# Performance work log

Measured on AMD Instinct MI355X. Metric: run time of the kernel, lower is better.

Reference implementation:

```python
import jax, jax.numpy as jnp
import numpy as np

EPS = 1e-08

def rotate_half(x):
    # split last dim into 2 halves: '... (j d) -> ... j d', j=2
    x1, x2 = jnp.split(x, 2, axis=-1)
    return jnp.concatenate((-x2, x1), axis=-1)

def apply_rotary_pos_emb(t, freqs):
    seq_len = t.shape[-2]
    freqs = freqs[:, :, -seq_len:]
    return t * jnp.cos(freqs) + rotate_half(t) * jnp.sin(freqs)

def setup_inputs() -> dict:
    key = jax.random.key(0)
    ks = jax.random.split(key, 6)
    B, N, D, H, DH = 2, 2048, 1024, 16, 64
    inner = H * DH
    x = jax.random.normal(ks[0], (B, N, D), dtype=jnp.float32)
    # realistic rotary frequencies over dim_head
    inv_freq = 1.0 / (10000.0 ** (np.arange(0, DH, 2, dtype=np.float32) / DH))
    t = np.arange(N, dtype=np.float32)
    freqs = np.einsum('n,f->nf', t, inv_freq)            # [N, DH/2]
    pos_emb = jnp.asarray(np.concatenate([freqs, freqs], axis=-1)[None, None])  # [1,1,N,DH]
    gamma = jnp.ones((D,), dtype=jnp.float32)
    Wq = jax.random.normal(ks[1], (D, inner), dtype=jnp.float32) * (D ** -0.5)
    Wkv = jax.random.normal(ks[2], (D, 2 * inner), dtype=jnp.float32) * (D ** -0.5)
    Wo = jax.random.normal(ks[3], (inner, D), dtype=jnp.float32) * (inner ** -0.5)
    bo = jnp.zeros((D,), dtype=jnp.float32)
    return {"x": x, "pos_emb": pos_emb, "gamma": gamma, "Wq": Wq, "Wkv": Wkv, "Wo": Wo, "bo": bo}

def reference(x, pos_emb, gamma, Wq, Wkv, Wo, bo):
    B, N, D = x.shape
    H = 16
    DH = Wq.shape[1] // H
    scale = DH ** -0.5
    # NOTE: kv_input is the UN-normalized x (captured before RMSNorm in the original)
    kv_input = x
    # RMSNorm: x / clamp(||x|| * dim^-0.5, eps) * gamma
    norm = jnp.linalg.norm(x, axis=-1, keepdims=True) * (D ** -0.5)
    xn = x / jnp.maximum(norm, EPS) * gamma
    q = xn @ Wq                                   # [B,N,H*DH]
    kv = kv_input @ Wkv
    k, v = jnp.split(kv, 2, axis=-1)
    def to_heads(t):
        return t.reshape(B, N, H, DH).transpose(0, 2, 1, 3)  # b h n d
    q, k, v = to_heads(q), to_heads(k), to_heads(v)
    q = q * scale
    q = apply_rotary_pos_emb(q, pos_emb)
    k = apply_rotary_pos_emb(k, pos_emb)
    sim = jnp.einsum('bhid,bhjd->bhij', q, k)
    i, j = sim.shape[-2:]
    causal_mask = jnp.triu(jnp.ones((i, j), dtype=bool), k=j - i + 1)
    mask_value = -jnp.finfo(sim.dtype).max
    sim = jnp.where(causal_mask, mask_value, sim)
    attn = jax.nn.softmax(sim, axis=-1)
    out = jnp.einsum('bhij,bhjd->bhid', attn, v)
    out = out.transpose(0, 2, 1, 3).reshape(B, N, H * DH)
    return out @ Wo + bo
```

## Files before the change

### kernel.cpp

```cpp
#include <hip/hip_runtime.h>
#include <cmath>

#define B_ 2
#define N_ 2048
#define D_ 1024
#define H_ 16

typedef __attribute__((ext_vector_type(8))) short short8;
typedef __attribute__((ext_vector_type(4))) float f32x4;
typedef __attribute__((ext_vector_type(4))) unsigned short u16x4;
typedef __attribute__((ext_vector_type(4))) unsigned int uint4v;

__device__ __forceinline__ unsigned short f2bf(float f) {
    union { float f; unsigned u; } x;
    x.f = f;
    unsigned r = x.u + 0x7FFFu + ((x.u >> 16) & 1u);
    return (unsigned short)(r >> 16);
}
__device__ __forceinline__ float bf2f(unsigned short u) {
    union { unsigned u; float f; } x;
    x.u = ((unsigned)u) << 16;
    return x.f;
}
__device__ __forceinline__ unsigned cvt_pk_bf16(float lo, float hi) {
    unsigned r;
    asm("v_cvt_pk_bf16_f32 %0, %1, %2" : "=v"(r) : "v"(lo), "v"(hi));
    return r;
}
__device__ __forceinline__ float exp2_fast(float x) {
    float r;
    asm("v_exp_f32 %0, %1" : "=v"(r) : "v"(x));
    return r;
}
__device__ __forceinline__ void gload_lds16(const void* g, void* l) {
    __builtin_amdgcn_global_load_lds((const __attribute__((address_space(1))) unsigned*)g,
                                     (__attribute__((address_space(3))) unsigned*)l,
                                     16, 0, 0);
}

__global__ __launch_bounds__(256) void freqtab_kernel(const float* __restrict__ pos,
                                                      float2* __restrict__ tabq,
                                                      float2* __restrict__ tabk) {
    const int idx = blockIdx.x * 256 + threadIdx.x;
    const float f = pos[idx];
    const float cc = cosf(f), ss = sinf(f);
    const float sq = 0.125f * 1.4426950408889634f;
    tabq[idx] = make_float2(sq * cc, sq * ss);
    tabk[idx] = make_float2(cc, ss);
}

__global__ __launch_bounds__(256) void rmsnorm_kernel(const float* __restrict__ x,
                                                      unsigned short* __restrict__ xb,
                                                      float* __restrict__ s) {
    const int row = blockIdx.x;
    const float4 v = reinterpret_cast<const float4*>(x + (size_t)row * D_)[threadIdx.x];
    float ss = v.x * v.x + v.y * v.y + v.z * v.z + v.w * v.w;
    #pragma unroll
    for (int off = 32; off; off >>= 1) ss += __shfl_xor(ss, off, 64);
    __shared__ float wss[4];
    if ((threadIdx.x & 63) == 0) wss[threadIdx.x >> 6] = ss;
    __syncthreads();
    const float tot = wss[0] + wss[1] + wss[2] + wss[3];
    const float inv = 1.0f / fmaxf(sqrtf(tot * (1.0f / D_)), 1e-8f);
    if (threadIdx.x == 0) s[row] = inv;
    u16x4 ox;
    ox[0] = f2bf(v.x); ox[1] = f2bf(v.y); ox[2] = f2bf(v.z); ox[3] = f2bf(v.w);
    *reinterpret_cast<u16x4*>(xb + (size_t)row * D_ + threadIdx.x * 4) = ox;
}

__global__ __launch_bounds__(256) void convT_all_kernel(const float* __restrict__ Wq,
                                                        const float* __restrict__ Wkv,
                                                        const float* __restrict__ Wo,
                                                        const float* __restrict__ gamma,
                                                        unsigned short* __restrict__ Wqt,
                                                        unsigned short* __restrict__ Wkvt,
                                                        unsigned short* __restrict__ Wot) {
    __shared__ float tile[32][33];
    const int bx = blockIdx.x;
    const float* W;
    unsigned short* Wt;
    int Nm, n0;
    bool gmul = false;
    if (bx < 32)       { W = Wq;  Wt = Wqt;  Nm = 1024; n0 = bx * 32; gmul = true; }
    else if (bx < 96)  { W = Wkv; Wt = Wkvt; Nm = 2048; n0 = (bx - 32) * 32; }
    else               { W = Wo;  Wt = Wot;  Nm = 1024; n0 = (bx - 96) * 32; }
    const int k0 = blockIdx.y * 32;
    const int r = threadIdx.x >> 3, c4 = (threadIdx.x & 7) * 4;
    const float4 ld = *reinterpret_cast<const float4*>(W + (size_t)(k0 + r) * Nm + n0 + c4);
    tile[r][c4 + 0] = ld.x; tile[r][c4 + 1] = ld.y;
    tile[r][c4 + 2] = ld.z; tile[r][c4 + 3] = ld.w;
    __syncthreads();
    u16x4 o;
    #pragma unroll
    for (int j = 0; j < 4; ++j) {
        float v = tile[c4 + j][r];
        if (gmul) v *= gamma[k0 + c4 + j];
        o[j] = f2bf(v);
    }
    *reinterpret_cast<u16x4*>(Wt + (size_t)(n0 + r) * 1024 + k0 + c4) = o;
}

__global__ __launch_bounds__(256) void gemm_qkv_kernel(const unsigned short* __restrict__ xb,
                                                       const unsigned short* __restrict__ Wqt,
                                                       const unsigned short* __restrict__ Wkvt,
                                                       const float* __restrict__ s,
                                                       unsigned short* __restrict__ qb,
                                                       unsigned short* __restrict__ kb,
                                                       unsigned short* __restrict__ vt,
                                                       const float2* __restrict__ tabq,
                                                       const float2* __restrict__ tabk) {
    __shared__ unsigned short As[2][64 * 64];
    __shared__ unsigned short Bs[2][128 * 64];
    __shared__ float sld[64];
    const int bid = blockIdx.x;
    const int xcd = bid & 7;
    const int ii = bid >> 3;
    const int bx = xcd * 3 + (ii % 3);
    const int m0 = (ii / 3) * 64;

    const unsigned short* Bt;
    int n0;
    if (bx < 8)       { Bt = Wqt;  n0 = bx * 128; }
    else if (bx < 16) { Bt = Wkvt; n0 = (bx - 8) * 128; }
    else              { Bt = Wkvt; n0 = (bx - 16) * 128 + 1024; }

    const int tid = threadIdx.x, lane = tid & 63, w = tid >> 6;
    const int wm = w >> 1, wn = w & 1;
    const int cc = lane & 15;
    const int sr = tid >> 3;
    const int sc = (tid & 7) * 8;

    if (tid < 64) sld[tid] = s[m0 + tid];

    f32x4 acc[2][4] = {};

    #pragma unroll
    for (int i = 0; i < 4; ++i) {
        const int r = i * 32 + sr;
        const int cs = sc ^ ((r & 7) << 3);
        if (i < 2)
            gload_lds16(xb + (size_t)(m0 + r) * 1024 + cs, (char*)As[0] + i * 4096 + w * 1024);
        gload_lds16(Bt + (size_t)(n0 + r) * 1024 + cs, (char*)Bs[0] + i * 4096 + w * 1024);
    }

    for (int t = 0; t < 16; ++t) {
        if (t + 1 < 16) {
            const int k0 = (t + 1) * 64;
            char* ad = (char*)As[(t + 1) & 1];
            char* bd = (char*)Bs[(t + 1) & 1];
            #pragma unroll
            for (int i = 0; i < 4; ++i) {
                const int r = i * 32 + sr;
                const int cs = sc ^ ((r & 7) << 3);
                if (i < 2)
                    gload_lds16(xb + (size_t)(m0 + r) * 1024 + k0 + cs, ad + i * 4096 + w * 1024);
                gload_lds16(Bt + (size_t)(n0 + r) * 1024 + k0 + cs, bd + i * 4096 + w * 1024);
            }
            asm volatile("s_waitcnt vmcnt(6)" ::: "memory");
        } else {
            asm volatile("s_waitcnt vmcnt(0)" ::: "memory");
        }
        __builtin_amdgcn_s_barrier();

        const char* Ac = (const char*)As[t & 1];
        const char* Bc = (const char*)Bs[t & 1];

        short8 af[2][2], bf[4][2];
        #pragma unroll
        for (int mf = 0; mf < 2; ++mf)
            #pragma unroll
            for (int ks = 0; ks < 2; ++ks) {
                const int r = wm * 32 + mf * 16 + cc;
                const int cb = (ks * 64 + ((lane >> 4) * 16)) ^ ((r & 7) << 4);
                af[mf][ks] = *reinterpret_cast<const short8*>(Ac + r * 128 + cb);
            }
        #pragma unroll
        for (int nf = 0; nf < 4; ++nf)
            #pragma unroll
            for (int ks = 0; ks < 2; ++ks) {
                const int r = wn * 64 + nf * 16 + cc;
                const int cb = (ks * 64 + ((lane >> 4) * 16)) ^ ((r & 7) << 4);
                bf[nf][ks] = *reinterpret_cast<const short8*>(Bc + r * 128 + cb);
            }
        #pragma unroll
        for (int ks = 0; ks < 2; ++ks)
            #pragma unroll
            for (int mf = 0; mf < 2; ++mf)
                #pragma unroll
                for (int nf = 0; nf < 4; ++nf)
                    acc[mf][nf] = __builtin_amdgcn_mfma_f32_16x16x32_bf16(af[mf][ks], bf[nf][ks], acc[mf][nf], 0, 0, 0);

        __builtin_amdgcn_s_barrier();
    }

    if (bx < 16) {
        const float2* tab = (bx < 8) ? tabq : tabk;
        unsigned short* dst = (bx < 8) ? qb : kb;
        const bool doscale = (bx < 8);
        #pragma unroll
        for (int mf = 0; mf < 2; ++mf)
            #pragma unroll
            for (int reg = 0; reg < 4; ++reg) {
                const int rloc = wm * 32 + mf * 16 + (lane >> 4) * 4 + reg;
                const int row = m0 + rloc;
                const int n = row & (N_ - 1);
                const float srow = doscale ? sld[rloc] : 1.0f;
                #pragma unroll
                for (int nf = 0; nf < 2; ++nf) {
                    const int d = nf * 16 + cc;
                    const float2 t1 = tab[n * 64 + d];
                    const float2 t2 = tab[n * 64 + 32 + d];
                    const float x1 = acc[mf][nf][reg] * srow;
                    const float x2 = acc[mf][nf + 2][reg] * srow;
                    const float o1 = x1 * t1.x - x2 * t1.y;
                    const float o2 = x2 * t2.x + x1 * t2.y;
                    const int col = n0 + wn * 64 + nf * 16 + cc;
                    dst[(size_t)row * 1024 + col] = f2bf(o1);
                    dst[(size_t)row * 1024 + col + 32] = f2bf(o2);
                }
            }
    } else {
        const int bb = m0 >> 11;
        const int gg = lane >> 4;
        const int tb = m0 & (N_ - 1);
        #pragma unroll
        for (int mf = 0; mf < 2; ++mf) {
            const int npos = tb + wm * 32 + (gg >> 1) * 16 + (gg & 1) * 8 + mf * 4;
            #pragma unroll
            for (int nf = 0; nf < 4; ++nf) {
                const int cv = n0 - 1024 + wn * 64 + nf * 16 + cc;
                const int h = cv >> 6, d = cv & 63;
                uint2 u;
                u.x = cvt_pk_bf16(acc[mf][nf][0], acc[mf][nf][1]);
                u.y = cvt_pk_bf16(acc[mf][nf][2], acc[mf][nf][3]);
                *reinterpret_cast<uint2*>(vt + ((size_t)(bb * 16 + h) * 64 + d) * 2048 + npos) = u;
            }
        }
    }
}

__global__ __launch_bounds__(256) void gemm_o_kernel(const unsigned short* __restrict__ A,
                                                     const unsigned short* __restrict__ Bt,
                                                     const float* __restrict__ bias,
                                                     float* __restrict__ Cout) {
    __shared__ unsigned short As[2][128 * 64];
    __shared__ unsigned short Bs[2][64 * 64];
    const int bid = blockIdx.x;
    const int xcd = bid & 7;
    const int ii = bid >> 3;
    const int n0 = (xcd * 2 + (ii & 1)) * 64;
    const int m0 = (ii >> 1) * 128;
    const int tid = threadIdx.x, lane = tid & 63, w = tid >> 6;
    const int wm = w >> 1, wn = w & 1;
    const int cc = lane & 15;
    const int sr = tid >> 3;
    const int sc = (tid & 7) * 8;

    f32x4 acc[4][2] = {};

    #pragma unroll
    for (int i = 0; i < 4; ++i) {
        const int r = i * 32 + sr;
        const int cs = sc ^ ((r & 7) << 3);
        gload_lds16(A + (size_t)(m0 + r) * 1024 + cs, (char*)As[0] + i * 4096 + w * 1024);
        if (i < 2)
            gload_lds16(Bt + (size_t)(n0 + r) * 1024 + cs, (char*)Bs[0] + i * 4096 + w * 1024);
    }

    for (int t = 0; t < 16; ++t) {
        if (t + 1 < 16) {
            const int k0 = (t + 1) * 64;
            char* ad = (char*)As[(t + 1) & 1];
            char* bd = (char*)Bs[(t + 1) & 1];
            #pragma unroll
            for (int i = 0; i < 4; ++i) {
                const int r = i * 32 + sr;
                const int cs = sc ^ ((r & 7) << 3);
                gload_lds16(A + (size_t)(m0 + r) * 1024 + k0 + cs, ad + i * 4096 + w * 1024);
                if (i < 2)
                    gload_lds16(Bt + (size_t)(n0 + r) * 1024 + k0 + cs, bd + i * 4096 + w * 1024);
            }
            asm volatile("s_waitcnt vmcnt(6)" ::: "memory");
        } else {
            asm volatile("s_waitcnt vmcnt(0)" ::: "memory");
        }
        __builtin_amdgcn_s_barrier();

        const char* Ac = (const char*)As[t & 1];
        const char* Bc = (const char*)Bs[t & 1];

        short8 af[4][2], bf[2][2];
        #pragma unroll
        for (int mf = 0; mf < 4; ++mf)
            #pragma unroll
            for (int ks = 0; ks < 2; ++ks) {
                const int r = wm * 64 + mf * 16 + cc;
                const int cb = (ks * 64 + ((lane >> 4) * 16)) ^ ((r & 7) << 4);
                af[mf][ks] = *reinterpret_cast<const short8*>(Ac + r * 128 + cb);
            }
        #pragma unroll
        for (int nf = 0; nf < 2; ++nf)
            #pragma unroll
            for (int ks = 0; ks < 2; ++ks) {
                const int r = wn * 32 + nf * 16 + cc;
                const int cb = (ks * 64 + ((lane >> 4) * 16)) ^ ((r & 7) << 4);
                bf[nf][ks] = *reinterpret_cast<const short8*>(Bc + r * 128 + cb);
            }
        #pragma unroll
        for (int ks = 0; ks < 2; ++ks)
            #pragma unroll
            for (int mf = 0; mf < 4; ++mf)
                #pragma unroll
                for (int nf = 0; nf < 2; ++nf)
                    acc[mf][nf] = __builtin_amdgcn_mfma_f32_16x16x32_bf16(af[mf][ks], bf[nf][ks], acc[mf][nf], 0, 0, 0);

        __builtin_amdgcn_s_barrier();
    }

    float bb[2];
    #pragma unroll
    for (int nf = 0; nf < 2; ++nf) bb[nf] = bias[n0 + wn * 32 + nf * 16 + cc];
    #pragma unroll
    for (int mf = 0; mf < 4; ++mf)
        #pragma unroll
        for (int nf = 0; nf < 2; ++nf)
            #pragma unroll
            for (int reg = 0; reg < 4; ++reg) {
                const int row = m0 + wm * 64 + mf * 16 + (lane >> 4) * 4 + reg;
                const int col = n0 + wn * 32 + nf * 16 + cc;
                Cout[(size_t)row * 1024 + col] = acc[mf][nf][reg] + bb[nf];
            }
}

__global__ __launch_bounds__(256, 6) void attn_mfma_kernel(const unsigned short* __restrict__ q,
                                                           const unsigned short* __restrict__ kb,
                                                           const unsigned short* __restrict__ vt,
                                                           unsigned short* __restrict__ att,
                                                           unsigned short* __restrict__ pO,
                                                           float2* __restrict__ pml) {
    const int bid = blockIdx.x;
    const int xcd = bid & 7;
    const int rest = bid >> 3;
    const int v = rest >> 5;
    const int u = rest & 31;
    const int a = u >> 4;
    const int p = u & 15;
    const int bh = xcd * 4 + 2 * a + (v & 1);
    const int s = (v >> 1) * 16 + ((v & 1) ? (15 - p) : p);
    int qi, t0, t1, half;
    bool split;
    if (s < 16) {
        qi = s; t0 = 0; t1 = qi + 1; half = 0; split = false;
    } else {
        const int qs = s - 16;
        qi = 16 + (qs >> 1);
        half = qs & 1;
        const int hmid = (qi + 2) >> 1;
        t0 = half ? hmid : 0;
        t1 = half ? (qi + 1) : hmid;
        split = true;
    }
    const int b = bh >> 4, h = bh & 15;
    const int qb_ = qi * 64;
    const int tid = threadIdx.x;
    const int lane = tid & 63;
    const int w = tid >> 6;
    const int c = lane & 15;
    const int g = lane >> 4;

    __shared__ __align__(16) unsigned short Ks[2][64 * 64];
    __shared__ __align__(16) unsigned short Vs[64 * 64];

    const int qrow = qb_ + w * 16 + c;
    short8 qf[2];
    {
        const unsigned short* qp = q + (size_t)(b * N_ + qrow) * 1024 + h * 64 + g * 8;
        qf[0] = *reinterpret_cast<const short8*>(qp);
        qf[1] = *reinterpret_cast<const short8*>(qp + 32);
    }

    float m = -1e30f, l = 0.f;
    f32x4 oacc[4] = {};

    const int sr = tid >> 3, sc = (tid & 7) * 8;
    const unsigned short* kbase = kb + (size_t)b * N_ * 1024 + h * 64;
    const unsigned short* vbase = vt + (size_t)bh * 64 * 2048;

    #pragma unroll
    for (int i = 0; i < 2; ++i) {
        const int r = i * 32 + sr;
        const int cs = sc ^ ((r & 7) << 3);
        gload_lds16(kbase + (size_t)(t0 * 64 + r) * 1024 + cs,
                    (char*)Ks[t0 & 1] + i * 4096 + w * 1024);
        gload_lds16(vbase + (size_t)r * 2048 + t0 * 64 + cs,
                    (char*)Vs + i * 4096 + w * 1024);
    }

    for (int t = t0; t < t1; ++t) {
        const int jb = t * 64;
        const int jn = jb + 64;
        if (t + 1 < t1) {
            char* kd = (char*)Ks[(t + 1) & 1];
            #pragma unroll
            for (int i = 0; i < 2; ++i) {
                const int r = i * 32 + sr;
                const int cs = sc ^ ((r & 7) << 3);
                gload_lds16(kbase + (size_t)(jn + r) * 1024 + cs, kd + i * 4096 + w * 1024);
            }
            asm volatile("s_waitcnt vmcnt(2)" ::: "memory");
        } else {
            asm volatile("s_waitcnt vmcnt(0)" ::: "memory");
        }
        __builtin_amdgcn_s_barrier();

        const char* Ksc = (const char*)Ks[t & 1];
        const char* Vsc = (const char*)Vs;

        f32x4 st[4];
        __builtin_amdgcn_s_setprio(1);
        #pragma unroll
        for (int ct = 0; ct < 4; ++ct) {
            const int key = ct * 16 + c;
            f32x4 acc = {0.f, 0.f, 0.f, 0.f};
            #pragma unroll
            for (int ks = 0; ks < 2; ++ks) {
                const int addr = (key * 128 + ks * 64 + g * 16) ^ ((key & 7) << 4);
                const short8 kf = *reinterpret_cast<const short8*>(Ksc + addr);
                acc = __builtin_amdgcn_mfma_f32_16x16x32_bf16(kf, qf[ks], acc, 0, 0, 0);
            }
            st[ct] = acc;
        }
        __builtin_amdgcn_s_setprio(0);

        float mx = -1e30f;
        if (jb + 63 > qrow) {
            #pragma unroll
            for (int ct = 0; ct < 4; ++ct)
                #pragma unroll
                for (int reg = 0; reg < 4; ++reg) {
                    const int key = jb + ct * 16 + g * 4 + reg;
                    const float sv = (key <= qrow) ? st[ct][reg] : -1e30f;
                    st[ct][reg] = sv;
                    mx = fmaxf(mx, sv);
                }
        } else {
            #pragma unroll
            for (int ct = 0; ct < 4; ++ct)
                mx = fmaxf(mx, fmaxf(fmaxf(st[ct][0], st[ct][1]),
                                     fmaxf(st[ct][2], st[ct][3])));
        }
        mx = fmaxf(mx, __shfl_xor(mx, 16, 64));
        mx = fmaxf(mx, __shfl_xor(mx, 32, 64));
        if (!__all(mx <= m + 8.0f)) {
            const float mn = fmaxf(m, mx);
            const float corr = exp2_fast(m - mn);
            l *= corr;
            m = mn;
            #pragma unroll
            for (int dt = 0; dt < 4; ++dt) {
                oacc[dt][0] *= corr; oacc[dt][1] *= corr;
                oacc[dt][2] *= corr; oacc[dt][3] *= corr;
            }
        }
        float rs = 0.f;
        #pragma unroll
        for (int ct = 0; ct < 4; ++ct)
            #pragma unroll
            for (int reg = 0; reg < 4; ++reg) {
                const float p2 = exp2_fast(st[ct][reg] - m);
                st[ct][reg] = p2;
                rs += p2;
            }
        rs += __shfl_xor(rs, 16, 64);
        rs += __shfl_xor(rs, 32, 64);
        l += rs;

        uint4v pv0, pv1;
        pv0[0] = cvt_pk_bf16(st[0][0], st[0][1]);
        pv0[1] = cvt_pk_bf16(st[0][2], st[0][3]);
        pv0[2] = cvt_pk_bf16(st[1][0], st[1][1]);
        pv0[3] = cvt_pk_bf16(st[1][2], st[1][3]);
        pv1[0] = cvt_pk_bf16(st[2][0], st[2][1]);
        pv1[1] = cvt_pk_bf16(st[2][2], st[2][3]);
        pv1[2] = cvt_pk_bf16(st[3][0], st[3][1]);
        pv1[3] = cvt_pk_bf16(st[3][2], st[3][3]);
        const short8 pf0 = *reinterpret_cast<const short8*>(&pv0);
        const short8 pf1 = *reinterpret_cast<const short8*>(&pv1);

        __builtin_amdgcn_s_setprio(1);
        #pragma unroll
        for (int dt = 0; dt < 4; ++dt) {
            const int vd = dt * 16 + c;
            {
                const int addr = (vd * 128 + 0 * 64 + g * 16) ^ ((vd & 7) << 4);
                const short8 vf = *reinterpret_cast<const short8*>(Vsc + addr);
                oacc[dt] = __builtin_amdgcn_mfma_f32_16x16x32_bf16(vf, pf0, oacc[dt], 0, 0, 0);
            }
            {
                const int addr = (vd * 128 + 1 * 64 + g * 16) ^ ((vd & 7) << 4);
                const short8 vf = *reinterpret_cast<const short8*>(Vsc + addr);
                oacc[dt] = __builtin_amdgcn_mfma_f32_16x16x32_bf16(vf, pf1, oacc[dt], 0, 0, 0);
            }
        }
        __builtin_amdgcn_s_setprio(0);

        __builtin_amdgcn_s_barrier();

        if (t + 1 < t1) {
            #pragma unroll
            for (int i = 0; i < 2; ++i) {
                const int r = i * 32 + sr;
                const int cs = sc ^ ((r & 7) << 3);
                gload_lds16(vbase + (size_t)r * 2048 + jn + cs, (char*)Vs + i * 4096 + w * 1024);
            }
        }
    }

    if (!split) {
        const float inv = 1.0f / l;
        unsigned short* orow = att + (size_t)(b * N_ + qrow) * 1024 + h * 64;
        #pragma unroll
        for (int dt = 0; dt < 4; ++dt) {
            #pragma unroll
            for (int rp = 0; rp < 2; ++rp) {
                const unsigned uu = cvt_pk_bf16(oacc[dt][2 * rp] * inv,
                                                oacc[dt][2 * rp + 1] * inv);
                *reinterpret_cast<unsigned*>(orow + dt * 16 + g * 4 + rp * 2) = uu;
            }
        }
    } else {
        const int slot = (bh * 16 + (qi - 16)) * 2 + half;
        const int rloc = w * 16 + c;
        pml[slot * 64 + rloc] = make_float2(m, l);
        unsigned short* prow = pO + (size_t)slot * 4096 + rloc * 64;
        #pragma unroll
        for (int dt = 0; dt < 4; ++dt) {
            #pragma unroll
            for (int rp = 0; rp < 2; ++rp) {
                const unsigned uu = cvt_pk_bf16(oacc[dt][2 * rp], oacc[dt][2 * rp + 1]);
                *reinterpret_cast<unsigned*>(prow + dt * 16 + g * 4 + rp * 2) = uu;
            }
        }
    }
}

__global__ __launch_bounds__(256) void attn_merge_kernel(const unsigned short* __restrict__ pO,
                                                         const float2* __restrict__ pml,
                                                         unsigned short* __restrict__ att) {
    const int blk = blockIdx.x;
    const int bh = blk >> 4;
    const int qt = blk & 15;
    const int qi = 16 + qt;
    const int b = bh >> 4, h = bh & 15;
    const int tid = threadIdx.x;
    const int row = tid >> 2;
    const int d0 = (tid & 3) * 16;
    const int slot0 = (bh * 16 + qt) * 2;
    const float2 ml0 = pml[slot0 * 64 + row];
    const float2 ml1 = pml[(slot0 + 1) * 64 + row];
    const float M = fmaxf(ml0.x, ml1.x);
    const float w0 = exp2_fast(ml0.x - M);
    const float w1 = exp2_fast(ml1.x - M);
    const float invL = 1.0f / (ml0.y * w0 + ml1.y * w1);
    const unsigned short* p0 = pO + (size_t)slot0 * 4096 + row * 64 + d0;
    const unsigned short* p1 = p0 + 4096;
    const int qrow = qi * 64 + row;
    unsigned short* orow = att + (size_t)(b * N_ + qrow) * 1024 + h * 64 + d0;
    #pragma unroll
    for (int j = 0; j < 16; j += 2) {
        const float a0 = (bf2f(p0[j]) * w0 + bf2f(p1[j]) * w1) * invL;
        const float a1 = (bf2f(p0[j + 1]) * w0 + bf2f(p1[j + 1]) * w1) * invL;
        *reinterpret_cast<unsigned*>(orow + j) = cvt_pk_bf16(a0, a1);
    }
}

extern "C" void kernel_launch(void* const* d_in, const int* in_sizes, int n_in,
                              void* d_out, int out_size, void* d_ws, size_t ws_size,
                              hipStream_t stream) {
    const float* x     = (const float*)d_in[0];
    const float* pos   = (const float*)d_in[1];
    const float* gamma = (const float*)d_in[2];
    const float* Wq    = (const float*)d_in[3];
    const float* Wkv   = (const float*)d_in[4];
    const float* Wo    = (const float*)d_in[5];
    const float* bo    = (const float*)d_in[6];
    float* out = (float*)d_out;
    char* ws = (char*)d_ws;

    const size_t MB = 1024 * 1024;
    unsigned short* kb   = (unsigned short*)(ws);
    unsigned short* qb   = (unsigned short*)(ws + 16 * MB);
    unsigned short* att  = (unsigned short*)(ws + 24 * MB);
    unsigned short* xb   = (unsigned short*)(ws + 32 * MB);
    unsigned short* Wqt  = (unsigned short*)(ws + 40 * MB);
    unsigned short* Wkvt = (unsigned short*)(ws + 42 * MB);
    unsigned short* Wot  = (unsigned short*)(ws + 46 * MB);
    unsigned short* vt   = (unsigned short*)(ws + 48 * MB);
    float2* tabq         = (float2*)(ws + 56 * MB);
    float2* tabk         = (float2*)(ws + 57 * MB);
    float* sv            = (float*)(ws + 58 * MB);
    unsigned short* pO   = (unsigned short*)(ws + 32 * MB);
    float2* pml          = (float2*)(ws + 40 * MB + 512 * 1024);

    freqtab_kernel<<<512, 256, 0, stream>>>(pos, tabq, tabk);
    convT_all_kernel<<<dim3(128, 32), 256, 0, stream>>>(Wq, Wkv, Wo, gamma, Wqt, Wkvt, Wot);
    rmsnorm_kernel<<<B_ * N_, 256, 0, stream>>>(x, xb, sv);

    gemm_qkv_kernel<<<1536, 256, 0, stream>>>(
        xb, Wqt, Wkvt, sv, qb, kb, vt, tabq, tabk);

    attn_mfma_kernel<<<1536, 256, 0, stream>>>(qb, kb, vt, att, pO, pml);
    attn_merge_kernel<<<512, 256, 0, stream>>>(pO, pml, att);

    gemm_o_kernel<<<512, 256, 0, stream>>>(att, Wot, bo, out);
}
```

Baseline: 113.5 us.

## Merge prologue kernels and single-buffer B tile in QKV GEMM for occupancy

Folds the frequency-table, weight-transpose and RMSNorm kernels into one prologue launch selected by block index, removing two kernel launches and their gaps. In the QKV GEMM the B tile drops from double to single buffering, with its next-tile load issued after the post-compute barrier, and launch bounds request 4 blocks per SM. This cuts LDS per block so more blocks can be resident, at the cost of exposing B-load latency at each iteration since the B prefetch now overlaps less with compute.

```diff
diff --git a/kernel.cpp b/kernel.cpp
--- a/kernel.cpp
+++ b/kernel.cpp
@@ -38,79 +38,80 @@
                                      16, 0, 0);
 }
 
-__global__ __launch_bounds__(256) void freqtab_kernel(const float* __restrict__ pos,
-                                                      float2* __restrict__ tabq,
-                                                      float2* __restrict__ tabk) {
-    const int idx = blockIdx.x * 256 + threadIdx.x;
-    const float f = pos[idx];
-    const float cc = cosf(f), ss = sinf(f);
-    const float sq = 0.125f * 1.4426950408889634f;
-    tabq[idx] = make_float2(sq * cc, sq * ss);
-    tabk[idx] = make_float2(cc, ss);
-}
-
-__global__ __launch_bounds__(256) void rmsnorm_kernel(const float* __restrict__ x,
-                                                      unsigned short* __restrict__ xb,
-                                                      float* __restrict__ s) {
-    const int row = blockIdx.x;
-    const float4 v = reinterpret_cast<const float4*>(x + (size_t)row * D_)[threadIdx.x];
-    float ss = v.x * v.x + v.y * v.y + v.z * v.z + v.w * v.w;
-    #pragma unroll
-    for (int off = 32; off; off >>= 1) ss += __shfl_xor(ss, off, 64);
+__global__ __launch_bounds__(256) void prologue_kernel(const float* __restrict__ x,
+                                                       const float* __restrict__ pos,
+                                                       const float* __restrict__ gamma,
+                                                       const float* __restrict__ Wq,
+                                                       const float* __restrict__ Wkv,
+                                                       const float* __restrict__ Wo,
+                                                       unsigned short* __restrict__ xb,
+                                                       float* __restrict__ s,
+                                                       float2* __restrict__ tabq,
+                                                       float2* __restrict__ tabk,
+                                                       unsigned short* __restrict__ Wqt,
+                                                       unsigned short* __restrict__ Wkvt,
+                                                       unsigned short* __restrict__ Wot) {
+    __shared__ float tile[32][33];
     __shared__ float wss[4];
-    if ((threadIdx.x & 63) == 0) wss[threadIdx.x >> 6] = ss;
-    __syncthreads();
-    const float tot = wss[0] + wss[1] + wss[2] + wss[3];
-    const float inv = 1.0f / fmaxf(sqrtf(tot * (1.0f / D_)), 1e-8f);
-    if (threadIdx.x == 0) s[row] = inv;
-    u16x4 ox;
-    ox[0] = f2bf(v.x); ox[1] = f2bf(v.y); ox[2] = f2bf(v.z); ox[3] = f2bf(v.w);
-    *reinterpret_cast<u16x4*>(xb + (size_t)row * D_ + threadIdx.x * 4) = ox;
-}
-
-__global__ __launch_bounds__(256) void convT_all_kernel(const float* __restrict__ Wq,
-                                                        const float* __restrict__ Wkv,
-                                                        const float* __restrict__ Wo,
-                                                        const float* __restrict__ gamma,
-                                                        unsigned short* __restrict__ Wqt,
-                                                        unsigned short* __restrict__ Wkvt,
-                                                        unsigned short* __restrict__ Wot) {
-    __shared__ float tile[32][33];
-    const int bx = blockIdx.x;
-    const float* W;
-    unsigned short* Wt;
-    int Nm, n0;
-    bool gmul = false;
-    if (bx < 32)       { W = Wq;  Wt = Wqt;  Nm = 1024; n0 = bx * 32; gmul = true; }
-    else if (bx < 96)  { W = Wkv; Wt = Wkvt; Nm = 2048; n0 = (bx - 32) * 32; }
-    else               { W = Wo;  Wt = Wot;  Nm = 1024; n0 = (bx - 96) * 32; }
-    const int k0 = blockIdx.y * 32;
-    const int r = threadIdx.x >> 3, c4 = (threadIdx.x & 7) * 4;
-    const float4 ld = *reinterpret_cast<const float4*>(W + (size_t)(k0 + r) * Nm + n0 + c4);
-    tile[r][c4 + 0] = ld.x; tile[r][c4 + 1] = ld.y;
-    tile[r][c4 + 2] = ld.z; tile[r][c4 + 3] = ld.w;
-    __syncthreads();
-    u16x4 o;
-    #pragma unroll
-    for (int j = 0; j < 4; ++j) {
-        float v = tile[c4 + j][r];
-        if (gmul) v *= gamma[k0 + c4 + j];
-        o[j] = f2bf(v);
-    }
-    *reinterpret_cast<u16x4*>(Wt + (size_t)(n0 + r) * 1024 + k0 + c4) = o;
-}
-
-__global__ __launch_bounds__(256) void gemm_qkv_kernel(const unsigned short* __restrict__ xb,
-                                                       const unsigned short* __restrict__ Wqt,
-                                                       const unsigned short* __restrict__ Wkvt,
-                                                       const float* __restrict__ s,
-                                                       unsigned short* __restrict__ qb,
-                                                       unsigned short* __restrict__ kb,
-                                                       unsigned short* __restrict__ vt,
-                                                       const float2* __restrict__ tabq,
-                                                       const float2* __restrict__ tabk) {
+    const int bid = blockIdx.x;
+    if (bid < 4096) {
+        const int bx = bid & 127;
+        const int k0 = (bid >> 7) * 32;
+        const float* W;
+        unsigned short* Wt;
+        int Nm, n0;
+        bool gmul = false;
+        if (bx < 32)       { W = Wq;  Wt = Wqt;  Nm = 1024; n0 = bx * 32; gmul = true; }
+        else if (bx < 96)  { W = Wkv; Wt = Wkvt; Nm = 2048; n0 = (bx - 32) * 32; }
+        else               { W = Wo;  Wt = Wot;  Nm = 1024; n0 = (bx - 96) * 32; }
+        const int r = threadIdx.x >> 3, c4 = (threadIdx.x & 7) * 4;
+        const float4 ld = *reinterpret_cast<const float4*>(W + (size_t)(k0 + r) * Nm + n0 + c4);
+        tile[r][c4 + 0] = ld.x; tile[r][c4 + 1] = ld.y;
+        tile[r][c4 + 2] = ld.z; tile[r][c4 + 3] = ld.w;
+        __syncthreads();
+        u16x4 o;
+        #pragma unroll
+        for (int j = 0; j < 4; ++j) {
+            float v = tile[c4 + j][r];
+            if (gmul) v *= gamma[k0 + c4 + j];
+            o[j] = f2bf(v);
+        }
+        *reinterpret_cast<u16x4*>(Wt + (size_t)(n0 + r) * 1024 + k0 + c4) = o;
+    } else if (bid < 8192) {
+        const int row = bid - 4096;
+        const float4 v = reinterpret_cast<const float4*>(x + (size_t)row * D_)[threadIdx.x];
+        float ss = v.x * v.x + v.y * v.y + v.z * v.z + v.w * v.w;
+        #pragma unroll
+        for (int off = 32; off; off >>= 1) ss += __shfl_xor(ss, off, 64);
+        if ((threadIdx.x & 63) == 0) wss[threadIdx.x >> 6] = ss;
+        __syncthreads();
+        const float tot = wss[0] + wss[1] + wss[2] + wss[3];
+        const float inv = 1.0f / fmaxf(sqrtf(tot * (1.0f / D_)), 1e-8f);
+        if (threadIdx.x == 0) s[row] = inv;
+        u16x4 ox;
+        ox[0] = f2bf(v.x); ox[1] = f2bf(v.y); ox[2] = f2bf(v.z); ox[3] = f2bf(v.w);
+        *reinterpret_cast<u16x4*>(xb + (size_t)row * D_ + threadIdx.x * 4) = ox;
+    } else {
+        const int idx = (bid - 8192) * 256 + threadIdx.x;
+        const float f = pos[idx];
+        const float cc = cosf(f), ssn = sinf(f);
+        const float sq = 0.125f * 1.4426950408889634f;
+        tabq[idx] = make_float2(sq * cc, sq * ssn);
+        tabk[idx] = make_float2(cc, ssn);
+    }
+}
+
+__global__ __launch_bounds__(256, 4) void gemm_qkv_kernel(const unsigned short* __restrict__ xb,
+                                                          const unsigned short* __restrict__ Wqt,
+                                                          const unsigned short* __restrict__ Wkvt,
+                                                          const float* __restrict__ s,
+                                                          unsigned short* __restrict__ qb,
+                                                          unsigned short* __restrict__ kb,
+                                                          unsigned short* __restrict__ vt,
+                                                          const float2* __restrict__ tabq,
+                                                          const float2* __restrict__ tabk) {
     __shared__ unsigned short As[2][64 * 64];
-    __shared__ unsigned short Bs[2][128 * 64];
+    __shared__ unsigned short Bs[128 * 64];
     __shared__ float sld[64];
     const int bid = blockIdx.x;
     const int xcd = bid & 7;
@@ -135,35 +136,36 @@
     f32x4 acc[2][4] = {};
 
     #pragma unroll
+    for (int i = 0; i < 2; ++i) {
+        const int r = i * 32 + sr;
+        const int cs = sc ^ ((r & 7) << 3);
+        gload_lds16(xb + (size_t)(m0 + r) * 1024 + cs, (char*)As[0] + i * 4096 + w * 1024);
+    }
+    #pragma unroll
     for (int i = 0; i < 4; ++i) {
         const int r = i * 32 + sr;
         const int cs = sc ^ ((r & 7) << 3);
-        if (i < 2)
-            gload_lds16(xb + (size_t)(m0 + r) * 1024 + cs, (char*)As[0] + i * 4096 + w * 1024);
-        gload_lds16(Bt + (size_t)(n0 + r) * 1024 + cs, (char*)Bs[0] + i * 4096 + w * 1024);
+        gload_lds16(Bt + (size_t)(n0 + r) * 1024 + cs, (char*)Bs + i * 4096 + w * 1024);
     }
 
     for (int t = 0; t < 16; ++t) {
         if (t + 1 < 16) {
             const int k0 = (t + 1) * 64;
             char* ad = (char*)As[(t + 1) & 1];
-            char* bd = (char*)Bs[(t + 1) & 1];
-            #pragma unroll
-            for (int i = 0; i < 4; ++i) {
+            #pragma unroll
+            for (int i = 0; i < 2; ++i) {
                 const int r = i * 32 + sr;
                 const int cs = sc ^ ((r & 7) << 3);
-                if (i < 2)
-                    gload_lds16(xb + (size_t)(m0 + r) * 1024 + k0 + cs, ad + i * 4096 + w * 1024);
-                gload_lds16(Bt + (size_t)(n0 + r) * 1024 + k0 + cs, bd + i * 4096 + w * 1024);
-            }
-            asm volatile("s_waitcnt vmcnt(6)" ::: "memory");
+                gload_lds16(xb + (size_t)(m0 + r) * 1024 + k0 + cs, ad + i * 4096 + w * 1024);
+            }
+            asm volatile("s_waitcnt vmcnt(2)" ::: "memory");
         } else {
             asm volatile("s_waitcnt vmcnt(0)" ::: "memory");
         }
         __builtin_amdgcn_s_barrier();
 
         const char* Ac = (const char*)As[t & 1];
-        const char* Bc = (const char*)Bs[t & 1];
+        const char* Bc = (const char*)Bs;
 
         short8 af[2][2], bf[4][2];
         #pragma unroll
@@ -191,6 +193,16 @@
                     acc[mf][nf] = __builtin_amdgcn_mfma_f32_16x16x32_bf16(af[mf][ks], bf[nf][ks], acc[mf][nf], 0, 0, 0);
 
         __builtin_amdgcn_s_barrier();
+
+        if (t + 1 < 16) {
+            const int k0 = (t + 1) * 64;
+            #pragma unroll
+            for (int i = 0; i < 4; ++i) {
+                const int r = i * 32 + sr;
+                const int cs = sc ^ ((r & 7) << 3);
+                gload_lds16(Bt + (size_t)(n0 + r) * 1024 + k0 + cs, (char*)Bs + i * 4096 + w * 1024);
+            }
+        }
     }
 
     if (bx < 16) {
@@ -602,9 +614,8 @@
     unsigned short* pO   = (unsigned short*)(ws + 32 * MB);
     float2* pml          = (float2*)(ws + 40 * MB + 512 * 1024);
 
-    freqtab_kernel<<<512, 256, 0, stream>>>(pos, tabq, tabk);
-    convT_all_kernel<<<dim3(128, 32), 256, 0, stream>>>(Wq, Wkv, Wo, gamma, Wqt, Wkvt, Wot);
-    rmsnorm_kernel<<<B_ * N_, 256, 0, stream>>>(x, xb, sv);
+    prologue_kernel<<<8704, 256, 0, stream>>>(
+        x, pos, gamma, Wq, Wkv, Wo, xb, sv, tabq, tabk, Wqt, Wkvt, Wot);
 
     gemm_qkv_kernel<<<1536, 256, 0, stream>>>(
         xb, Wqt, Wkvt, sv, qb, kb, vt, tabq, tabk);
```

After: 106.1 us. 6.6% less time.
